# Kernel optimization log

Hardware: AMD Instinct MI355X
Metric: run time of the kernel (lower is better)

## Reference

```python
import jax, jax.numpy as jnp
import numpy as np

LEN_M = 131328   # (data_dim+1) * d_h = 513 * 256
D_H = 256
N_MC = 64
DATA_DIM_P1 = 513
N = 4096


def setup_inputs() -> dict:
    key = jax.random.key(0)
    k1, k2, k3, k4 = jax.random.split(key, 4)
    params = jax.random.normal(k1, (2 * LEN_M,), dtype=jnp.float32)
    W1 = jax.random.normal(k2, (D_H + 1,), dtype=jnp.float32)
    x = jax.random.normal(k3, (N, DATA_DIM_P1), dtype=jnp.float32)
    eps = jax.random.normal(k4, (N_MC,), dtype=jnp.float32)
    return {"params": params, "W1": W1, "x": x, "eps": eps}


def reference(params, W1, x, eps):
    # split variational params into means and (relu'd) variances
    m_w0 = params[:LEN_M]                                  # [len_m]
    v_w0 = jax.nn.relu(params[LEN_M:]) + 1e-6              # [len_m]
    # reparameterized MC sampling; NOTE: torch code draws ONE scalar eps per
    # MC sample (randn(m_w0[0].shape) is scalar), shared across all weights.
    samps_w0 = m_w0[:, None] + eps[None, :] * jnp.sqrt(v_w0)[:, None]  # [len_m, M]
    W0 = samps_w0.reshape(DATA_DIM_P1, D_H, N_MC)          # [d+1, h, M]
    # fused batched GEMM replacing the d_h * num_MC_samps tiny matmuls
    x_w0 = jnp.einsum('nd,dhm->nhm', x, W0)                # [N, h, M]
    z = jax.nn.relu(x_w0)
    ones = jnp.ones((x.shape[0], 1, N_MC), dtype=x.dtype)
    z = jnp.concatenate([ones, z], axis=1)                 # [N, h+1, M]
    pred_samps = jnp.einsum('nhm,h->nm', z, W1)            # [N, M]
    return pred_samps, m_w0, v_w0
```

## Files before the change

kernel.cpp:

```cpp
#include <hip/hip_runtime.h>
#include <hip/hip_bf16.h>
#include <math.h>

#define LEN_M   131328
#define D_H     256
#define N_MC    64
#define D_P1    513
#define NROW    4096
#define KPAD    512
#define PRED_ELEMS (NROW * N_MC)

#define XB_ELEMS   (NROW * KPAD)
#define WCBT_ELEMS (512 * 512)

typedef __attribute__((ext_vector_type(8))) short short8;
typedef __attribute__((ext_vector_type(4))) float floatx4;

__global__ __launch_bounds__(256) void prep_a(
    const float* __restrict__ params, const float* __restrict__ x,
    float* __restrict__ out, __hip_bfloat16* __restrict__ xb,
    float* __restrict__ wcl)
{
    int i = blockIdx.x * 256 + threadIdx.x;
    int row = i >> 9, col = i & 511;
    xb[i] = __float2bfloat16(x[row * D_P1 + col]);
    if (i < PRED_ELEMS) out[i] = 0.0f;
    if (i < LEN_M) {
        float m = params[i];
        float v = fmaxf(params[LEN_M + i], 0.0f) + 1e-6f;
        out[PRED_ELEMS + i]         = m;
        out[PRED_ELEMS + LEN_M + i] = v;
        if (i >= 131072) {
            int h = i - 131072;
            wcl[h]       = m;
            wcl[256 + h] = sqrtf(v);
        }
    }
}

__global__ __launch_bounds__(256) void prep_b(
    const float* __restrict__ params, __hip_bfloat16* __restrict__ wcbt)
{
    __shared__ unsigned short T[64][65];
    const int k0 = blockIdx.x * 64;
    const int c0 = blockIdx.y * 64;
    const int t  = threadIdx.x;
    const int hh = t & 63, kb = t >> 6;
    const bool spart = (c0 >= 256);
    const int hbase = c0 & 255;
    const float* src = params + (spart ? LEN_M : 0);

    #pragma unroll 4
    for (int p = 0; p < 16; ++p) {
        int kk = p * 4 + kb;
        float v = src[(k0 + kk) * 256 + hbase + hh];
        if (spart) v = sqrtf(fmaxf(v, 0.0f) + 1e-6f);
        __hip_bfloat16 b = __float2bfloat16(v);
        T[kk][hh] = *(unsigned short*)&b;
    }
    __syncthreads();

    const int cc = t >> 2, kq = t & 3;
    short8 lo, hi;
    #pragma unroll
    for (int j = 0; j < 8; ++j) lo[j] = (short)T[kq * 16 + j][cc];
    #pragma unroll
    for (int j = 0; j < 8; ++j) hi[j] = (short)T[kq * 16 + 8 + j][cc];
    short* dst = (short*)wcbt + (c0 + cc) * 512 + k0 + kq * 16;
    *(short8*)dst       = lo;
    *(short8*)(dst + 8) = hi;
}

__global__ __launch_bounds__(256) void main_kernel(
    const __hip_bfloat16* __restrict__ xb, const __hip_bfloat16* __restrict__ wcbt,
    const float* __restrict__ wcl, const float* __restrict__ x,
    const float* __restrict__ W1, const float* __restrict__ eps,
    float* __restrict__ out)
{
    __shared__ float Clds[128 * 36];

    const int t = threadIdx.x;
    const int w = t >> 6, lane = t & 63;
    const int lane15 = lane & 15, quad = lane >> 4;
    const int H  = blockIdx.x;
    const int bm = blockIdx.y * 32;
    const int rowhalf = (w & 1) * 16;
    const int colhalf = w >> 1;

    const int arow  = bm + rowhalf + lane15;
    const int gcol0 = colhalf * 256 + H * 64 + lane15;

    const short* xbs = (const short*)xb;
    const short* wbs = (const short*)wcbt;
    const short* ap  = xbs + arow * 512 + quad * 8;
    const short* bp0 = wbs + (gcol0 +  0) * 512 + quad * 8;
    const short* bp1 = wbs + (gcol0 + 16) * 512 + quad * 8;
    const short* bp2 = wbs + (gcol0 + 32) * 512 + quad * 8;
    const short* bp3 = wbs + (gcol0 + 48) * 512 + quad * 8;

    floatx4 acc0 = {0.f,0.f,0.f,0.f}, acc1 = acc0, acc2 = acc0, acc3 = acc0;

    #pragma unroll 4
    for (int k0 = 0; k0 < 512; k0 += 32) {
        short8 a  = *(const short8*)(ap  + k0);
        short8 b0 = *(const short8*)(bp0 + k0);
        short8 b1 = *(const short8*)(bp1 + k0);
        short8 b2 = *(const short8*)(bp2 + k0);
        short8 b3 = *(const short8*)(bp3 + k0);
        acc0 = __builtin_amdgcn_mfma_f32_16x16x32_bf16(a, b0, acc0, 0, 0, 0);
        acc1 = __builtin_amdgcn_mfma_f32_16x16x32_bf16(a, b1, acc1, 0, 0, 0);
        acc2 = __builtin_amdgcn_mfma_f32_16x16x32_bf16(a, b2, acc2, 0, 0, 0);
        acc3 = __builtin_amdgcn_mfma_f32_16x16x32_bf16(a, b3, acc3, 0, 0, 0);
    }

    const int r0 = rowhalf + quad * 4;
    float xl[4];
    #pragma unroll
    for (int r = 0; r < 4; ++r) xl[r] = x[(bm + r0 + r) * D_P1 + 512];

    floatx4 accs[4] = {acc0, acc1, acc2, acc3};
    #pragma unroll
    for (int s = 0; s < 4; ++s) {
        const int gcol = gcol0 + s * 16;
        const float wl = wcl[gcol];
        float4 vv;
        vv.x = accs[s][0] + xl[0] * wl;
        vv.y = accs[s][1] + xl[1] * wl;
        vv.z = accs[s][2] + xl[2] * wl;
        vv.w = accs[s][3] + xl[3] * wl;
        const int lcol = colhalf * 64 + s * 16 + lane15;
        *(float4*)&Clds[lcol * 36 + r0] = vv;
    }
    __syncthreads();

    const float e = eps[lane];
    const int rb = w * 8;
    float accp[8];
    const float init = (H == 0) ? W1[0] : 0.0f;
    #pragma unroll
    for (int r = 0; r < 8; ++r) accp[r] = init;

    #pragma unroll 4
    for (int hl = 0; hl < 64; ++hl) {
        const float w1h = W1[1 + H * 64 + hl];
        const float4 a0 = *(const float4*)&Clds[hl * 36 + rb];
        const float4 a1 = *(const float4*)&Clds[hl * 36 + rb + 4];
        const float4 b0 = *(const float4*)&Clds[(64 + hl) * 36 + rb];
        const float4 b1 = *(const float4*)&Clds[(64 + hl) * 36 + rb + 4];
        accp[0] = fmaf(fmaxf(fmaf(e, b0.x, a0.x), 0.f), w1h, accp[0]);
        accp[1] = fmaf(fmaxf(fmaf(e, b0.y, a0.y), 0.f), w1h, accp[1]);
        accp[2] = fmaf(fmaxf(fmaf(e, b0.z, a0.z), 0.f), w1h, accp[2]);
        accp[3] = fmaf(fmaxf(fmaf(e, b0.w, a0.w), 0.f), w1h, accp[3]);
        accp[4] = fmaf(fmaxf(fmaf(e, b1.x, a1.x), 0.f), w1h, accp[4]);
        accp[5] = fmaf(fmaxf(fmaf(e, b1.y, a1.y), 0.f), w1h, accp[5]);
        accp[6] = fmaf(fmaxf(fmaf(e, b1.z, a1.z), 0.f), w1h, accp[6]);
        accp[7] = fmaf(fmaxf(fmaf(e, b1.w, a1.w), 0.f), w1h, accp[7]);
    }

    float* op = out + (bm + rb) * 64 + lane;
    #pragma unroll
    for (int r = 0; r < 8; ++r)
        unsafeAtomicAdd(op + r * 64, accp[r]);
}

extern "C" void kernel_launch(void* const* d_in, const int* in_sizes, int n_in,
                              void* d_out, int out_size, void* d_ws, size_t ws_size,
                              hipStream_t stream)
{
    const float* params = (const float*)d_in[0];
    const float* W1     = (const float*)d_in[1];
    const float* x      = (const float*)d_in[2];
    const float* eps    = (const float*)d_in[3];
    float* out = (float*)d_out;

    __hip_bfloat16* xb   = (__hip_bfloat16*)d_ws;
    __hip_bfloat16* wcbt = xb + XB_ELEMS;
    float*          wcl  = (float*)(wcbt + WCBT_ELEMS);

    prep_a<<<XB_ELEMS / 256, 256, 0, stream>>>(params, x, out, xb, wcl);
    prep_b<<<dim3(8, 8), 256, 0, stream>>>(params, wcbt);
    main_kernel<<<dim3(4, 128), 256, 0, stream>>>(xb, wcbt, wcl, x, W1, eps, out);
}
```

Baseline: 98.90 us.

## Merge prep kernels into one launch and halve main kernel row tile

The two preprocessing kernels become one launch whose block index picks the role: the first 8192 blocks do the conversion and copy, the last 64 do the weight transpose. This removes one kernel launch and the gap between launches. The main kernel now handles 16 rows per block instead of 32, with each wave computing two MFMA tiles instead of four, which doubles the grid to 1024 blocks for more parallelism across CUs. In exchange, every weight column tile is loaded twice as often in total and the number of atomic adds per output stays the same, but spread over more blocks.

```diff
diff --git a/kernel.cpp b/kernel.cpp
--- a/kernel.cpp
+++ b/kernel.cpp
@@ -16,35 +16,37 @@
 typedef __attribute__((ext_vector_type(8))) short short8;
 typedef __attribute__((ext_vector_type(4))) float floatx4;
 
-__global__ __launch_bounds__(256) void prep_a(
+__global__ __launch_bounds__(256) void prep_kernel(
     const float* __restrict__ params, const float* __restrict__ x,
     float* __restrict__ out, __hip_bfloat16* __restrict__ xb,
-    float* __restrict__ wcl)
-{
-    int i = blockIdx.x * 256 + threadIdx.x;
-    int row = i >> 9, col = i & 511;
-    xb[i] = __float2bfloat16(x[row * D_P1 + col]);
-    if (i < PRED_ELEMS) out[i] = 0.0f;
-    if (i < LEN_M) {
-        float m = params[i];
-        float v = fmaxf(params[LEN_M + i], 0.0f) + 1e-6f;
-        out[PRED_ELEMS + i]         = m;
-        out[PRED_ELEMS + LEN_M + i] = v;
-        if (i >= 131072) {
-            int h = i - 131072;
-            wcl[h]       = m;
-            wcl[256 + h] = sqrtf(v);
-        }
-    }
-}
-
-__global__ __launch_bounds__(256) void prep_b(
-    const float* __restrict__ params, __hip_bfloat16* __restrict__ wcbt)
+    float* __restrict__ wcl, __hip_bfloat16* __restrict__ wcbt)
 {
     __shared__ unsigned short T[64][65];
-    const int k0 = blockIdx.x * 64;
-    const int c0 = blockIdx.y * 64;
-    const int t  = threadIdx.x;
+    const int bid = blockIdx.x;
+    const int t   = threadIdx.x;
+
+    if (bid < 8192) {
+        int i = bid * 256 + t;
+        int row = i >> 9, col = i & 511;
+        xb[i] = __float2bfloat16(x[row * D_P1 + col]);
+        if (i < PRED_ELEMS) out[i] = 0.0f;
+        if (i < LEN_M) {
+            float m = params[i];
+            float v = fmaxf(params[LEN_M + i], 0.0f) + 1e-6f;
+            out[PRED_ELEMS + i]         = m;
+            out[PRED_ELEMS + LEN_M + i] = v;
+            if (i >= 131072) {
+                int h = i - 131072;
+                wcl[h]       = m;
+                wcl[256 + h] = sqrtf(v);
+            }
+        }
+        return;
+    }
+
+    const int b2 = bid - 8192;
+    const int k0 = (b2 & 7) * 64;
+    const int c0 = (b2 >> 3) * 64;
     const int hh = t & 63, kb = t >> 6;
     const bool spart = (c0 >= 256);
     const int hbase = c0 & 255;
@@ -77,89 +79,72 @@
     const float* __restrict__ W1, const float* __restrict__ eps,
     float* __restrict__ out)
 {
-    __shared__ float Clds[128 * 36];
+    __shared__ float Clds[128 * 20];
 
     const int t = threadIdx.x;
     const int w = t >> 6, lane = t & 63;
     const int lane15 = lane & 15, quad = lane >> 4;
     const int H  = blockIdx.x;
-    const int bm = blockIdx.y * 32;
-    const int rowhalf = (w & 1) * 16;
-    const int colhalf = w >> 1;
+    const int bm = blockIdx.y * 16;
 
-    const int arow  = bm + rowhalf + lane15;
-    const int gcol0 = colhalf * 256 + H * 64 + lane15;
+    const int part  = w >> 1;
+    const int sub   = (w & 1) * 32;
+    const int lcol0 = part * 64 + sub;
+    const int gc0   = part * 256 + H * 64 + sub + lane15;
 
-    const short* xbs = (const short*)xb;
-    const short* wbs = (const short*)wcbt;
-    const short* ap  = xbs + arow * 512 + quad * 8;
-    const short* bp0 = wbs + (gcol0 +  0) * 512 + quad * 8;
-    const short* bp1 = wbs + (gcol0 + 16) * 512 + quad * 8;
-    const short* bp2 = wbs + (gcol0 + 32) * 512 + quad * 8;
-    const short* bp3 = wbs + (gcol0 + 48) * 512 + quad * 8;
+    const float e = eps[lane];
+    const int r0 = quad * 4;
+    float xl[4];
+    #pragma unroll
+    for (int r = 0; r < 4; ++r) xl[r] = x[(bm + r0 + r) * D_P1 + 512];
 
-    floatx4 acc0 = {0.f,0.f,0.f,0.f}, acc1 = acc0, acc2 = acc0, acc3 = acc0;
+    const short* ap  = (const short*)xb   + (bm + lane15) * 512 + quad * 8;
+    const short* bp0 = (const short*)wcbt + (gc0 +  0) * 512 + quad * 8;
+    const short* bp1 = (const short*)wcbt + (gc0 + 16) * 512 + quad * 8;
+
+    floatx4 acc0 = {0.f,0.f,0.f,0.f}, acc1 = acc0;
 
     #pragma unroll 4
     for (int k0 = 0; k0 < 512; k0 += 32) {
         short8 a  = *(const short8*)(ap  + k0);
         short8 b0 = *(const short8*)(bp0 + k0);
         short8 b1 = *(const short8*)(bp1 + k0);
-        short8 b2 = *(const short8*)(bp2 + k0);
-        short8 b3 = *(const short8*)(bp3 + k0);
         acc0 = __builtin_amdgcn_mfma_f32_16x16x32_bf16(a, b0, acc0, 0, 0, 0);
         acc1 = __builtin_amdgcn_mfma_f32_16x16x32_bf16(a, b1, acc1, 0, 0, 0);
-        acc2 = __builtin_amdgcn_mfma_f32_16x16x32_bf16(a, b2, acc2, 0, 0, 0);
-        acc3 = __builtin_amdgcn_mfma_f32_16x16x32_bf16(a, b3, acc3, 0, 0, 0);
     }
 
-    const int r0 = rowhalf + quad * 4;
-    float xl[4];
+    floatx4 accs[2] = {acc0, acc1};
     #pragma unroll
-    for (int r = 0; r < 4; ++r) xl[r] = x[(bm + r0 + r) * D_P1 + 512];
-
-    floatx4 accs[4] = {acc0, acc1, acc2, acc3};
-    #pragma unroll
-    for (int s = 0; s < 4; ++s) {
-        const int gcol = gcol0 + s * 16;
-        const float wl = wcl[gcol];
+    for (int s = 0; s < 2; ++s) {
+        const float wl = wcl[gc0 + s * 16];
         float4 vv;
         vv.x = accs[s][0] + xl[0] * wl;
         vv.y = accs[s][1] + xl[1] * wl;
         vv.z = accs[s][2] + xl[2] * wl;
         vv.w = accs[s][3] + xl[3] * wl;
-        const int lcol = colhalf * 64 + s * 16 + lane15;
-        *(float4*)&Clds[lcol * 36 + r0] = vv;
+        const int lcol = lcol0 + s * 16 + lane15;
+        *(float4*)&Clds[lcol * 20 + r0] = vv;
     }
     __syncthreads();
 
-    const float e = eps[lane];
-    const int rb = w * 8;
-    float accp[8];
+    const int rb = w * 4;
     const float init = (H == 0) ? W1[0] : 0.0f;
-    #pragma unroll
-    for (int r = 0; r < 8; ++r) accp[r] = init;
+    float accp[4] = {init, init, init, init};
 
-    #pragma unroll 4
+    #pragma unroll 8
     for (int hl = 0; hl < 64; ++hl) {
         const float w1h = W1[1 + H * 64 + hl];
-        const float4 a0 = *(const float4*)&Clds[hl * 36 + rb];
-        const float4 a1 = *(const float4*)&Clds[hl * 36 + rb + 4];
-        const float4 b0 = *(const float4*)&Clds[(64 + hl) * 36 + rb];
-        const float4 b1 = *(const float4*)&Clds[(64 + hl) * 36 + rb + 4];
+        const float4 a0 = *(const float4*)&Clds[hl * 20 + rb];
+        const float4 b0 = *(const float4*)&Clds[(64 + hl) * 20 + rb];
         accp[0] = fmaf(fmaxf(fmaf(e, b0.x, a0.x), 0.f), w1h, accp[0]);
         accp[1] = fmaf(fmaxf(fmaf(e, b0.y, a0.y), 0.f), w1h, accp[1]);
         accp[2] = fmaf(fmaxf(fmaf(e, b0.z, a0.z), 0.f), w1h, accp[2]);
         accp[3] = fmaf(fmaxf(fmaf(e, b0.w, a0.w), 0.f), w1h, accp[3]);
-        accp[4] = fmaf(fmaxf(fmaf(e, b1.x, a1.x), 0.f), w1h, accp[4]);
-        accp[5] = fmaf(fmaxf(fmaf(e, b1.y, a1.y), 0.f), w1h, accp[5]);
-        accp[6] = fmaf(fmaxf(fmaf(e, b1.z, a1.z), 0.f), w1h, accp[6]);
-        accp[7] = fmaf(fmaxf(fmaf(e, b1.w, a1.w), 0.f), w1h, accp[7]);
     }
 
     float* op = out + (bm + rb) * 64 + lane;
     #pragma unroll
-    for (int r = 0; r < 8; ++r)
+    for (int r = 0; r < 4; ++r)
         unsafeAtomicAdd(op + r * 64, accp[r]);
 }
 
@@ -177,7 +162,6 @@
     __hip_bfloat16* wcbt = xb + XB_ELEMS;
     float*          wcl  = (float*)(wcbt + WCBT_ELEMS);
 
-    prep_a<<<XB_ELEMS / 256, 256, 0, stream>>>(params, x, out, xb, wcl);
-    prep_b<<<dim3(8, 8), 256, 0, stream>>>(params, wcbt);
-    main_kernel<<<dim3(4, 128), 256, 0, stream>>>(xb, wcbt, wcl, x, W1, eps, out);
+    prep_kernel<<<8192 + 64, 256, 0, stream>>>(params, x, out, xb, wcl, wcbt);
+    main_kernel<<<dim3(4, 256), 256, 0, stream>>>(xb, wcbt, wcl, x, W1, eps, out);
 }
```

Result: no change. 99.98 us (+1.1%).
